# Performance work log

Measured on AMD Instinct MI355X. Metric: run time of the kernel, lower is better.

Reference implementation:

```python
import jax, jax.numpy as jnp
import numpy as np

B, IN, U = 16, 1024, 1024


def _wSw(W, S):
    # W: [i,u], S: [b,i,i] -> W^T S W : [b,u,u]
    return jnp.einsum('iu,bij,jv->buv', W, S, W)


def _xSx(x, Wsig):
    # (sum_i x_i^2) * W_Sigma, broadcast over batch
    return jnp.sum(x * x, axis=1)[:, None, None] * Wsig


def _trS(S, Wsig):
    return jnp.trace(S, axis1=1, axis2=2)[:, None, None] * Wsig


def _hadamard_sigma(s1, s2, m1, m2):
    # s1*s2 + diag(m1) s2 diag(m1) + diag(m2) s1 diag(m2)
    return (s1 * s2
            + m1[:, :, None] * s2 * m1[:, None, :]
            + m2[:, :, None] * s1 * m2[:, None, :])


def _act_sigma(g, S):
    # S * outer(g, g)
    return S * (g[:, :, None] * g[:, None, :])


def setup_inputs() -> dict:
    key = jax.random.key(0)
    ks = jax.random.split(key, 16)
    f32 = jnp.float32
    init_mu, ini_sigma = 0.05, -4.6
    inp = {
        'mu_inputs': jax.random.normal(ks[0], (B, IN), f32),
        'sigma_inputs': 0.01 * jax.random.normal(ks[1], (B, IN, IN), f32),
        'prev_state': 0.1 * jax.random.normal(ks[2], (B, U), f32),
        'Sigma_state': 0.01 * jax.random.normal(ks[3], (B, U, U), f32),
        'U_z': init_mu * jax.random.normal(ks[4], (IN, U), f32),
        'uz_sigma': jnp.full((U,), ini_sigma, f32),
        'W_z': init_mu * jax.random.normal(ks[5], (U, U), f32),
        'wz_sigma': jnp.full((U,), ini_sigma, f32),
        'U_r': init_mu * jax.random.normal(ks[6], (IN, U), f32),
        'ur_sigma': jnp.full((U,), ini_sigma, f32),
        'W_r': init_mu * jax.random.normal(ks[7], (U, U), f32),
        'wr_sigma': jnp.full((U,), ini_sigma, f32),
        'U_h': init_mu * jax.random.normal(ks[8], (IN, U), f32),
        'uh_sigma': jnp.full((U,), ini_sigma, f32),
        'W_h': init_mu * jax.random.normal(ks[9], (U, U), f32),
        'wh_sigma': jnp.full((U,), ini_sigma, f32),
    }
    return inp


def reference(mu_inputs, sigma_inputs, prev_state, Sigma_state,
              U_z, uz_sigma, W_z, wz_sigma,
              U_r, ur_sigma, W_r, wr_sigma,
              U_h, uh_sigma, W_h, wh_sigma):
    sp = jax.nn.softplus
    # ---- z gate ----
    pre_z = mu_inputs @ U_z + prev_state @ W_z
    z = jax.nn.sigmoid(pre_z)
    Uz_S, Wz_S = jnp.diag(sp(uz_sigma)), jnp.diag(sp(wz_sigma))
    Sigma_zz = (_wSw(U_z, sigma_inputs) + _xSx(mu_inputs, Uz_S) + _trS(sigma_inputs, Uz_S)
                + _wSw(W_z, Sigma_state) + _xSx(prev_state, Wz_S) + _trS(Sigma_state, Wz_S))
    Sigma_z = _act_sigma(z * (1.0 - z), Sigma_zz)  # analytic d sigmoid
    # ---- r gate ----
    pre_r = mu_inputs @ U_r + prev_state @ W_r
    r = jax.nn.sigmoid(pre_r)
    Ur_S, Wr_S = jnp.diag(sp(ur_sigma)), jnp.diag(sp(wr_sigma))
    Sigma_rr = (_wSw(U_r, sigma_inputs) + _xSx(mu_inputs, Ur_S) + _trS(sigma_inputs, Ur_S)
                + _wSw(W_r, Sigma_state) + _xSx(prev_state, Wr_S) + _trS(Sigma_state, Wr_S))
    Sigma_r = _act_sigma(r * (1.0 - r), Sigma_rr)
    # ---- h gate ----
    sr = prev_state * r
    pre_h = mu_inputs @ U_h + sr @ W_h
    h = jnp.tanh(pre_h)
    Uh_S, Wh_S = jnp.diag(sp(uh_sigma)), jnp.diag(sp(wh_sigma))
    sigma_g = _hadamard_sigma(Sigma_state, Sigma_r, prev_state, r)
    Sigma_hh = (_wSw(U_h, sigma_inputs) + _xSx(mu_inputs, Uh_S) + _trS(sigma_inputs, Uh_S)
                + _wSw(W_h, sigma_g) + _xSx(sr, Wh_S) + _trS(sigma_g, Wh_S))
    Sigma_h = _act_sigma(1.0 - h * h, Sigma_hh)  # analytic d tanh
    # ---- combine ----
    mu_out = z * prev_state + (1.0 - z) * h
    sigma_a = _hadamard_sigma(Sigma_z, Sigma_state, z, prev_state)
    sigma_b = _hadamard_sigma(Sigma_z, Sigma_h, 1.0 - z, h)
    sigma_ab = Sigma_z * (prev_state[:, :, None] * h[:, None, :])
    sigma_abT = Sigma_z * (h[:, :, None] * prev_state[:, None, :])
    Sigma_out = sigma_a + sigma_b - sigma_ab - sigma_abT
    Sigma_out = jnp.where(jnp.isfinite(Sigma_out), Sigma_out, jnp.zeros_like(Sigma_out))
    eye = jnp.eye(Sigma_out.shape[-1], dtype=bool)
    Sigma_out = jnp.where(eye, jnp.abs(Sigma_out), Sigma_out)
    return mu_out, Sigma_out
```

## Files before the change

kernel.cpp:

```cpp
#include <hip/hip_runtime.h>
#include <math.h>


#define B_  16
#define N_  1024
#define NN_ (1024*1024)

typedef __bf16 bf16x8 __attribute__((ext_vector_type(8)));
typedef float  f32x4  __attribute__((ext_vector_type(4)));
typedef unsigned short ushort8v __attribute__((ext_vector_type(8)));

__device__ __forceinline__ unsigned short f2bf(float f) {
  union { float f; unsigned int u; } v; v.f = f;
  unsigned int r = v.u + 0x7fffu + ((v.u >> 16) & 1u);
  return (unsigned short)(r >> 16);
}
__device__ __forceinline__ float bf2f(unsigned short h) {
  union { unsigned int u; float f; } v; v.u = ((unsigned int)h) << 16;
  return v.f;
}
__device__ __forceinline__ float f4get(const float4& v, int q) {
  return q == 0 ? v.x : (q == 1 ? v.y : (q == 2 ? v.z : v.w));
}
__device__ __forceinline__ unsigned short u4get(const ushort4& v, int q) {
  return q == 0 ? v.x : (q == 1 ? v.y : (q == 2 ? v.z : v.w));
}

__device__ __forceinline__ void gload_lds16(const void* g, void* l) {
  __builtin_amdgcn_global_load_lds((__attribute__((address_space(1))) void*)g,
                                   (__attribute__((address_space(3))) void*)l,
                                   16, 0, 0);
}

template<int OMODE, int PAIR>
__global__ __launch_bounds__(512)
void gemm256(const unsigned short* __restrict__ A, int lda, long aStride, int koffA,
             const unsigned short* __restrict__ Bm, const unsigned short* __restrict__ Bm2,
             int ldb, long bStride, int K,
             void* __restrict__ Out, int ldo, long oStride, int noff,
             const float* __restrict__ act,
             const float* __restrict__ spU, const float* __restrict__ spW,
             const float* __restrict__ dU, const float* __restrict__ dW)
{
  __shared__ unsigned short lds[65536];
  const int b = blockIdx.z;
  const unsigned short* Bsel = Bm;
  int nofx = noff, nbx = blockIdx.x;
  if (PAIR) {
    const int half = gridDim.x >> 1;
    if (nbx >= half) { Bsel = Bm2; nofx = 1024; nbx -= half; }
  }
  const int nbase = nbx * 256;
  const int mbase = blockIdx.y * 256;
  const int t = threadIdx.x, lane = t & 63, w = t >> 6;
  const int wm = w >> 2, wn = w & 3;
  const int NT = K >> 5;

  f32x4 acc[8][4];
  const f32x4 zero4 = {0.f, 0.f, 0.f, 0.f};
#pragma unroll
  for (int i = 0; i < 8; i++)
#pragma unroll
    for (int j = 0; j < 4; j++) acc[i][j] = zero4;

  const int l3 = lane >> 3, l7 = lane & 7;
  const int posg = l7 ^ l3;
  const int gr = ((w * 8 + l3) << 1) + (posg >> 2);
  const int gc = (posg & 3) << 3;
  const unsigned short* Ag = A + (size_t)b * aStride + (size_t)(mbase + gr) * lda + koffA + gc;
  const unsigned short* Bg = Bsel + (size_t)b * bStride + (size_t)(nbase + gr) * ldb + gc;
  const size_t a128 = (size_t)128 * lda, bb128 = (size_t)128 * ldb;
  char* ldsb = (char*)lds;
  const int wdst = w << 10;

  const int lrow = lane & 15, c4 = lane >> 4;
  const int aoff = ((lrow >> 1) << 7) + ((((((lrow & 1) << 2) | c4)) ^ (lrow >> 1)) << 4);
  const int abase0 = (wm << 13);
  const int bbase0 = 16384 + (wn << 12);

  auto STAGE = [&](int kt) {
    const int p = kt & 3;
    const size_t ko = (size_t)kt << 5;
    char* base = ldsb + (p << 15);
    gload_lds16(Ag + ko,          base + wdst);
    gload_lds16(Ag + ko + a128,   base + 8192  + wdst);
    gload_lds16(Bg + ko,          base + 16384 + wdst);
    gload_lds16(Bg + ko + bb128,  base + 24576 + wdst);
  };
  auto LDA8 = [&](const char* pbuf, int mi) -> bf16x8 {
    return *(const bf16x8*)(pbuf + abase0 + (mi << 10) + aoff);
  };
  auto LDB8 = [&](const char* pbuf, int ni) -> bf16x8 {
    return *(const bf16x8*)(pbuf + bbase0 + (ni << 10) + aoff);
  };

  STAGE(0); STAGE(1);
  asm volatile("s_waitcnt vmcnt(4)" ::: "memory");
  __builtin_amdgcn_sched_barrier(0);
  __builtin_amdgcn_s_barrier();
  __builtin_amdgcn_sched_barrier(0);

  bf16x8 a0[4], a1[4], b0[2], b1[2];
#pragma unroll
  for (int i = 0; i < 4; i++) a0[i] = LDA8(ldsb, i);
#pragma unroll
  for (int i = 0; i < 2; i++) b0[i] = LDB8(ldsb, i);

  for (int kt = 0; kt < NT; ++kt) {
    const char* pbuf = ldsb + ((size_t)(kt & 3) << 15);
    const char* pnxt = ldsb + ((size_t)((kt + 1) & 3) << 15);
#pragma unroll
    for (int i = 0; i < 2; i++) b1[i] = LDB8(pbuf, 2 + i);
#pragma unroll
    for (int ni = 0; ni < 2; ni++)
#pragma unroll
      for (int mi = 0; mi < 4; mi++)
        acc[mi][ni] = __builtin_amdgcn_mfma_f32_16x16x32_bf16(a0[mi], b0[ni], acc[mi][ni], 0, 0, 0);
#pragma unroll
    for (int i = 0; i < 4; i++) a1[i] = LDA8(pbuf, 4 + i);
#pragma unroll
    for (int ni = 0; ni < 2; ni++)
#pragma unroll
      for (int mi = 0; mi < 4; mi++)
        acc[mi][2 + ni] = __builtin_amdgcn_mfma_f32_16x16x32_bf16(a0[mi], b1[ni], acc[mi][2 + ni], 0, 0, 0);
    if (kt + 2 < NT) {
      STAGE(kt + 2);
      asm volatile("s_waitcnt vmcnt(4)" ::: "memory");
    } else {
      asm volatile("s_waitcnt vmcnt(0)" ::: "memory");
    }
    __builtin_amdgcn_sched_barrier(0);
    __builtin_amdgcn_s_barrier();
    __builtin_amdgcn_sched_barrier(0);
    if (kt + 1 < NT) {
#pragma unroll
      for (int i = 0; i < 4; i++) a0[i] = LDA8(pnxt, i);
    }
#pragma unroll
    for (int ni = 0; ni < 2; ni++)
#pragma unroll
      for (int mi = 0; mi < 4; mi++)
        acc[4 + mi][ni] = __builtin_amdgcn_mfma_f32_16x16x32_bf16(a1[mi], b0[ni], acc[4 + mi][ni], 0, 0, 0);
    if (kt + 1 < NT) {
#pragma unroll
      for (int i = 0; i < 2; i++) b0[i] = LDB8(pnxt, i);
    }
#pragma unroll
    for (int ni = 0; ni < 2; ni++)
#pragma unroll
      for (int mi = 0; mi < 4; mi++)
        acc[4 + mi][2 + ni] = __builtin_amdgcn_mfma_f32_16x16x32_bf16(a1[mi], b1[ni], acc[4 + mi][2 + ni], 0, 0, 0);
  }

  if (OMODE == 2) {
    const float* actb = act + b * N_;
    const float dUb = dU[b], dWb = dW[b];
#pragma unroll
    for (int mi = 0; mi < 8; mi++) {
      const int u0 = mbase + wm * 128 + mi * 16 + ((lane >> 4) << 2);
#pragma unroll
      for (int ni = 0; ni < 4; ni++) {
        const int v = nbase + wn * 64 + ni * 16 + (lane & 15);
        const float avv = actb[v];
#pragma unroll
        for (int r = 0; r < 4; r++) {
          const int u = u0 + r;
          float val = acc[mi][ni][r];
          if (u == v) val += dUb * spU[u] + dWb * spW[u];
          val *= actb[u] * avv;
          ((float*)Out)[(size_t)b * oStride + (size_t)u * ldo + v] = val;
        }
      }
    }
  } else {
    __syncthreads();
    unsigned short* reg = lds + w * 8192;
    const float* actb = (OMODE == 1) ? (act + b * N_) : nullptr;
    float dUb = 0.f, dWb = 0.f;
    if (OMODE == 1) { dUb = dU[b]; dWb = dW[b]; }
#pragma unroll
    for (int mi = 0; mi < 8; mi++) {
      const int rl0 = mi * 16 + ((lane >> 4) << 2);
#pragma unroll
      for (int ni = 0; ni < 4; ni++) {
        const int cl = ni * 16 + (lane & 15);
#pragma unroll
        for (int r = 0; r < 4; r++) {
          const int rl = rl0 + r;
          float val = acc[mi][ni][r];
          if (OMODE == 1) {
            const int u = mbase + wm * 128 + rl, v = nbase + wn * 64 + cl;
            if (u == v) val += dUb * spU[u] + dWb * spW[u];
            val *= actb[u] * actb[v];
          }
          reg[rl * 64 + cl] = f2bf(val);
        }
      }
    }
    unsigned short* obase = (unsigned short*)Out + (size_t)b * oStride
        + (size_t)(mbase + wm * 128) * ldo + nofx + nbase + wn * 64;
#pragma unroll
    for (int pp = 0; pp < 16; pp++) {
      const int row = pp * 8 + (lane >> 3);
      const int ch = lane & 7;
      ushort8v vv = *(const ushort8v*)&reg[row * 64 + ch * 8];
      *(ushort8v*)(obase + (size_t)row * ldo + ch * 8) = vv;
    }
  }
}


__global__ void conv_bf16(const float* __restrict__ in, unsigned short* __restrict__ out, int n4)
{
  int i = blockIdx.x * 256 + threadIdx.x;
  const int stride = gridDim.x * 256;
  for (; i < n4; i += stride) {
    const float4 v = ((const float4*)in)[i];
    ushort4 o;
    o.x = f2bf(v.x); o.y = f2bf(v.y); o.z = f2bf(v.z); o.w = f2bf(v.w);
    ((ushort4*)out)[i] = o;
  }
}

__global__ void build_AT(const float* __restrict__ Uz, const float* __restrict__ Wz,
                         const float* __restrict__ Ur, const float* __restrict__ Wr,
                         const float* __restrict__ Uh, const float* __restrict__ Wh,
                         unsigned short* __restrict__ AT)
{
  __shared__ float tile[32][33];
  const int g = blockIdx.z;
  const float* U = g == 0 ? Uz : (g == 1 ? Ur : Uh);
  const float* W = g == 0 ? Wz : (g == 1 ? Wr : Wh);
  const int u0  = blockIdx.x * 32;
  const int k0g = blockIdx.y * 32;
  const float* src = (k0g >= 1024) ? W : U;
  const int kloc = k0g & 1023;
  const int tx = threadIdx.x & 31, ty = threadIdx.x >> 5;
  unsigned short* out = AT + (size_t)g * N_ * 2048;
#pragma unroll
  for (int i = 0; i < 32; i += 8) tile[ty + i][tx] = src[(size_t)(kloc + ty + i) * N_ + u0 + tx];
  __syncthreads();
#pragma unroll
  for (int i = 0; i < 32; i += 8)
    out[(size_t)(u0 + ty + i) * 2048 + k0g + tx] = f2bf(tile[tx][ty + i]);
}

__global__ void softplus6(const float* a0, const float* a1, const float* a2,
                          const float* a3, const float* a4, const float* a5,
                          float* __restrict__ sp)
{
  const float* src[6] = {a0, a1, a2, a3, a4, a5};
  const int g = blockIdx.x;
  const float* s = src[g];
  for (int i = threadIdx.x; i < N_; i += 256) {
    float x = s[i];
    sp[g * N_ + i] = (x > 20.f) ? x : log1pf(expf(x));
  }
}

__global__ void scalars1(const float* __restrict__ mu, const float* __restrict__ prev,
                         const float* __restrict__ sin_, const float* __restrict__ Sst,
                         float* __restrict__ dA, float* __restrict__ dBzr)
{
  __shared__ float red[256];
  const int b = blockIdx.x;
  float s1 = 0.f, s2 = 0.f;
  for (int i = threadIdx.x; i < N_; i += 256) {
    const float m = mu[b * N_ + i];
    s1 += m * m + sin_[(size_t)b * NN_ + (size_t)i * (N_ + 1)];
    const float p = prev[b * N_ + i];
    s2 += p * p + Sst[(size_t)b * NN_ + (size_t)i * (N_ + 1)];
  }
  red[threadIdx.x] = s1; __syncthreads();
  for (int s = 128; s > 0; s >>= 1) { if (threadIdx.x < s) red[threadIdx.x] += red[threadIdx.x + s]; __syncthreads(); }
  if (threadIdx.x == 0) dA[b] = red[0];
  __syncthreads();
  red[threadIdx.x] = s2; __syncthreads();
  for (int s = 128; s > 0; s >>= 1) { if (threadIdx.x < s) red[threadIdx.x] += red[threadIdx.x + s]; __syncthreads(); }
  if (threadIdx.x == 0) dBzr[b] = red[0];
}

__global__ __launch_bounds__(256)
void gate_pre2(const float* __restrict__ x1, const float* __restrict__ x2,
               const float* __restrict__ U0, const float* __restrict__ W0,
               const float* __restrict__ U1, const float* __restrict__ W1,
               float* __restrict__ Ppart)
{
  const int g  = blockIdx.z;
  const int ks = blockIdx.y;
  const int out = blockIdx.x * 256 + threadIdx.x;
  const int b = out >> 10, col = out & 1023;
  const float* x = (ks < 4) ? x1 : x2;
  const float* Wm = (g == 0) ? ((ks < 4) ? U0 : W0) : ((ks < 4) ? U1 : W1);
  const int k0 = (ks & 3) * 256;
  const float* xb = x + b * N_ + k0;
  const float* wp = Wm + (size_t)k0 * N_ + col;
  float acc = 0.f;
#pragma unroll 8
  for (int k = 0; k < 256; k++)
    acc += xb[k] * wp[(size_t)k * N_];
  Ppart[(g * 8 + ks) * (B_ * N_) + out] = acc;
}

__global__ void gate_act2(const float* __restrict__ P,
                          float* __restrict__ z, float* __restrict__ gz,
                          float* __restrict__ r, float* __restrict__ gr)
{
  const int out = blockIdx.x * 256 + threadIdx.x;
  float a0 = 0.f, a1 = 0.f;
#pragma unroll
  for (int ks = 0; ks < 8; ks++) {
    a0 += P[ks * (B_ * N_) + out];
    a1 += P[(8 + ks) * (B_ * N_) + out];
  }
  const float s0 = 1.f / (1.f + expf(-a0));
  const float s1 = 1.f / (1.f + expf(-a1));
  z[out] = s0; gz[out] = s0 * (1.f - s0);
  r[out] = s1; gr[out] = s1 * (1.f - s1);
}

__global__ __launch_bounds__(256)
void gate_pre1(const float* __restrict__ x1, const float* __restrict__ x2,
               const float* __restrict__ U0, const float* __restrict__ W0,
               float* __restrict__ Ppart)
{
  const int ks = blockIdx.y;
  const int out = blockIdx.x * 256 + threadIdx.x;
  const int b = out >> 10, col = out & 1023;
  const float* x = (ks < 4) ? x1 : x2;
  const float* Wm = (ks < 4) ? U0 : W0;
  const int k0 = (ks & 3) * 256;
  const float* xb = x + b * N_ + k0;
  const float* wp = Wm + (size_t)k0 * N_ + col;
  float acc = 0.f;
#pragma unroll 8
  for (int k = 0; k < 256; k++)
    acc += xb[k] * wp[(size_t)k * N_];
  Ppart[ks * (B_ * N_) + out] = acc;
}

__global__ void gate_act1(const float* __restrict__ P,
                          float* __restrict__ h, float* __restrict__ gh)
{
  const int out = blockIdx.x * 256 + threadIdx.x;
  float a0 = 0.f;
#pragma unroll
  for (int ks = 0; ks < 8; ks++) a0 += P[ks * (B_ * N_) + out];
  const float s = tanhf(a0);
  h[out] = s; gh[out] = 1.f - s * s;
}

__global__ void sr_csr(const float* __restrict__ prev, const float* __restrict__ r,
                       float* __restrict__ sr, float* __restrict__ csr)
{
  __shared__ float red[256];
  const int b = blockIdx.x;
  float s = 0.f;
  for (int i = threadIdx.x; i < N_; i += 256) {
    const float v = prev[b * N_ + i] * r[b * N_ + i];
    sr[b * N_ + i] = v;
    s += v * v;
  }
  red[threadIdx.x] = s; __syncthreads();
  for (int k = 128; k > 0; k >>= 1) { if (threadIdx.x < k) red[threadIdx.x] += red[threadIdx.x + k]; __syncthreads(); }
  if (threadIdx.x == 0) csr[b] = red[0];
}

__global__ void hadamard_sg(const float* __restrict__ Sst, unsigned short* __restrict__ Sg,
                            const float* __restrict__ prev, const float* __restrict__ r)
{
  const size_t idx = ((size_t)blockIdx.x * 256 + threadIdx.x) * 4;
  const int b = (int)(idx >> 20);
  const int rem = (int)(idx & (NN_ - 1));
  const int i = rem >> 10, j0 = rem & 1023;
  const float pi = prev[b * N_ + i], ri = r[b * N_ + i];
  const float4  ss  = *(const float4*)(Sst + (size_t)b * NN_ + rem);
  const ushort4 sr4 = *(const ushort4*)(Sg + (size_t)b * NN_ + rem);
  ushort4 o;
  unsigned short* op = (unsigned short*)&o;
#pragma unroll
  for (int q = 0; q < 4; q++) {
    const float srv = bf2f(u4get(sr4, q));
    const float stv = f4get(ss, q);
    const float pj = prev[b * N_ + j0 + q];
    const float rj = r[b * N_ + j0 + q];
    op[q] = f2bf(stv * srv + pi * pj * srv + ri * rj * stv);
  }
  *(ushort4*)(Sg + (size_t)b * NN_ + rem) = o;
}

__global__ void scalars2(const unsigned short* __restrict__ Sg,
                         const float* __restrict__ csr, float* __restrict__ dBh)
{
  __shared__ float red[256];
  const int b = blockIdx.x;
  float s = 0.f;
  for (int i = threadIdx.x; i < N_; i += 256)
    s += bf2f(Sg[(size_t)b * NN_ + (size_t)i * (N_ + 1)]);
  red[threadIdx.x] = s; __syncthreads();
  for (int k = 128; k > 0; k >>= 1) { if (threadIdx.x < k) red[threadIdx.x] += red[threadIdx.x + k]; __syncthreads(); }
  if (threadIdx.x == 0) dBh[b] = red[0] + csr[b];
}

__global__ void mu_kernel(const float* __restrict__ z, const float* __restrict__ prev,
                          const float* __restrict__ h, float* __restrict__ mu_out)
{
  const int i = blockIdx.x * 256 + threadIdx.x;
  const float zz = z[i];
  mu_out[i] = zz * prev[i] + (1.f - zz) * h[i];
}

__global__ void combine(const unsigned short* __restrict__ Sz, const float* __restrict__ Sst,
                        const float* __restrict__ z, const float* __restrict__ prev,
                        const float* __restrict__ h, float* __restrict__ SigOut)
{
  const int row = blockIdx.x;
  const int b = row >> 10, u = row & 1023;
  const float zu = z[b * N_ + u], pu = prev[b * N_ + u], hu = h[b * N_ + u];
  const size_t base = (size_t)b * NN_ + (size_t)u * N_;
  const int j0 = threadIdx.x * 4;
  const ushort4 s4 = *(const ushort4*)(Sz + base + j0);
  const float4 sh = *(const float4*)(SigOut + base + j0);
  const float4 st = *(const float4*)(Sst + base + j0);
  const float4 zv = *(const float4*)(z + b * N_ + j0);
  const float4 pv = *(const float4*)(prev + b * N_ + j0);
  const float4 hv = *(const float4*)(h + b * N_ + j0);
  float o[4];
#pragma unroll
  for (int q = 0; q < 4; q++) {
    const int v = j0 + q;
    const float sz  = bf2f(u4get(s4, q));
    const float shh = f4get(sh, q);
    const float stt = f4get(st, q);
    const float zvv = f4get(zv, q);
    const float pvv = f4get(pv, q);
    const float hvv = f4get(hv, q);
    float res = sz * stt + zu * zvv * stt + pu * pvv * sz
              + sz * shh + (1.f - zu) * (1.f - zvv) * shh + hu * hvv * sz
              - sz * (pu * hvv) - sz * (hu * pvv);
    if (!isfinite(res)) res = 0.f;
    if (u == v) res = fabsf(res);
    o[q] = res;
  }
  float4 ov; ov.x = o[0]; ov.y = o[1]; ov.z = o[2]; ov.w = o[3];
  *(float4*)(SigOut + base + j0) = ov;
}


extern "C" void kernel_launch(void* const* d_in, const int* in_sizes, int n_in,
                              void* d_out, int out_size, void* d_ws, size_t ws_size,
                              hipStream_t stream)
{
  const float* mu   = (const float*)d_in[0];
  const float* sin_ = (const float*)d_in[1];
  const float* prev = (const float*)d_in[2];
  const float* Sst  = (const float*)d_in[3];
  const float* Uz = (const float*)d_in[4];  const float* uzs = (const float*)d_in[5];
  const float* Wz = (const float*)d_in[6];  const float* wzs = (const float*)d_in[7];
  const float* Ur = (const float*)d_in[8];  const float* urs = (const float*)d_in[9];
  const float* Wr = (const float*)d_in[10]; const float* wrs = (const float*)d_in[11];
  const float* Uh = (const float*)d_in[12]; const float* uhs = (const float*)d_in[13];
  const float* Wh = (const float*)d_in[14]; const float* whs = (const float*)d_in[15];

  char* ws = (char*)d_ws;
  size_t off = 0;
  auto take = [&](size_t bytes) -> char* {
    char* p = ws + off;
    off = (off + bytes + 255) & ~(size_t)255;
    return p;
  };
  unsigned short* Tcm = (unsigned short*)take((size_t)B_ * 2048 * 1024 * 2);
  unsigned short* Sz  = (unsigned short*)take((size_t)B_ * NN_ * 2);
  unsigned short* Sg  = (unsigned short*)take((size_t)B_ * NN_ * 2);
  unsigned short* AT  = (unsigned short*)take((size_t)3 * N_ * 2048 * 2);
  float* Ppart = (float*)take((size_t)16 * B_ * N_ * 4);
  float* sp   = (float*)take(6 * N_ * 4);
  float* z    = (float*)take(B_ * N_ * 4);
  float* gz   = (float*)take(B_ * N_ * 4);
  float* rr   = (float*)take(B_ * N_ * 4);
  float* gr   = (float*)take(B_ * N_ * 4);
  float* h    = (float*)take(B_ * N_ * 4);
  float* gh   = (float*)take(B_ * N_ * 4);
  float* sr   = (float*)take(B_ * N_ * 4);
  float* dA   = (float*)take(64);
  float* dBzr = (float*)take(64);
  float* dBh  = (float*)take(64);
  float* csr  = (float*)take(64);
  if (off > ws_size) return;

  float* mu_out = (float*)d_out;
  float* SigOut = (float*)d_out + (size_t)B_ * N_;
  unsigned short* SinH = (unsigned short*)SigOut;
  unsigned short* SstH = (unsigned short*)SigOut + (size_t)B_ * NN_;

  const unsigned short* ATz = AT;
  const unsigned short* ATr = AT + (size_t)N_ * 2048;
  const unsigned short* ATh = AT + (size_t)2 * N_ * 2048;

  conv_bf16<<<2048, 256, 0, stream>>>(sin_, SinH, B_ * NN_ / 4);
  conv_bf16<<<2048, 256, 0, stream>>>(Sst,  SstH, B_ * NN_ / 4);
  softplus6<<<6, 256, 0, stream>>>(uzs, wzs, urs, wrs, uhs, whs, sp);
  scalars1<<<16, 256, 0, stream>>>(mu, prev, sin_, Sst, dA, dBzr);
  build_AT<<<dim3(32, 64, 3), 256, 0, stream>>>(Uz, Wz, Ur, Wr, Uh, Wh, AT);
  gate_pre2<<<dim3(64, 8, 2), 256, 0, stream>>>(mu, prev, Uz, Wz, Ur, Wr, Ppart);
  gate_act2<<<64, 256, 0, stream>>>(Ppart, z, gz, rr, gr);
  sr_csr<<<16, 256, 0, stream>>>(prev, rr, sr, csr);
  gate_pre1<<<dim3(64, 8), 256, 0, stream>>>(mu, sr, Uh, Wh, Ppart);
  gate_act1<<<64, 256, 0, stream>>>(Ppart, h, gh);

  const dim3 gg1(8, 4, 16);
  const dim3 gg2(4, 4, 16);
  const long tS = (long)2048 * 1024;

  gemm256<0, 1><<<gg1, 512, 0, stream>>>(ATz, 2048, 0, 0, SinH, SstH, 1024, (long)NN_, 1024,
                                         Tcm, 2048, tS, 0, nullptr, nullptr, nullptr, nullptr, nullptr);
  gemm256<1, 0><<<gg2, 512, 0, stream>>>(ATz, 2048, 0, 0, Tcm, nullptr, 2048, tS, 2048,
                                         Sz, 1024, (long)NN_, 0, gz, sp + 0, sp + 1024, dA, dBzr);
  gemm256<0, 1><<<gg1, 512, 0, stream>>>(ATr, 2048, 0, 0, SinH, SstH, 1024, (long)NN_, 1024,
                                         Tcm, 2048, tS, 0, nullptr, nullptr, nullptr, nullptr, nullptr);
  gemm256<1, 0><<<gg2, 512, 0, stream>>>(ATr, 2048, 0, 0, Tcm, nullptr, 2048, tS, 2048,
                                         Sg, 1024, (long)NN_, 0, gr, sp + 2048, sp + 3072, dA, dBzr);
  hadamard_sg<<<16384, 256, 0, stream>>>(Sst, Sg, prev, rr);
  scalars2<<<16, 256, 0, stream>>>(Sg, csr, dBh);
  gemm256<0, 1><<<gg1, 512, 0, stream>>>(ATh, 2048, 0, 0, SinH, Sg, 1024, (long)NN_, 1024,
                                         Tcm, 2048, tS, 0, nullptr, nullptr, nullptr, nullptr, nullptr);
  gemm256<2, 0><<<gg2, 512, 0, stream>>>(ATh, 2048, 0, 0, Tcm, nullptr, 2048, tS, 2048,
                                         SigOut, 1024, (long)NN_, 0, gh, sp + 4096, sp + 5120, dA, dBh);
  mu_kernel<<<64, 256, 0, stream>>>(z, prev, h, mu_out);
  combine<<<16384, 256, 0, stream>>>(Sz, Sst, z, prev, h, SigOut);
}
```

Before: 584.7 us.

## Rewrite batched GEMM as an 8-phase ping-pong pipeline with XCD-aware block mapping

Replaces the 4-stage, K=32 GEMM with a double-buffered, K=64 tile using 128KB of LDS. Each tile is split into four MFMA phases that interleave LDS reads and half-tile global loads, with barriers and s_setprio around the MFMA bursts. It also switches to a 1D grid that maps panels across XCDs for cache locality, and adds an XOR swizzle to the bf16 epilogue staging to reduce LDS bank conflicts. The paired mode now also offsets the A column by 1024 for the second half, which changes which half of the packed weights multiplies the state covariance. The larger LDS footprint limits occupancy to one block per CU.

```diff
diff --git a/kernel.cpp b/kernel.cpp
--- a/kernel.cpp
+++ b/kernel.cpp
@@ -32,29 +32,33 @@
                                    16, 0, 0);
 }
 
+#define MFMA_ __builtin_amdgcn_mfma_f32_16x16x32_bf16
+
 template<int OMODE, int PAIR>
 __global__ __launch_bounds__(512)
-void gemm256(const unsigned short* __restrict__ A, int lda, long aStride, int koffA,
-             const unsigned short* __restrict__ Bm, const unsigned short* __restrict__ Bm2,
-             int ldb, long bStride, int K,
-             void* __restrict__ Out, int ldo, long oStride, int noff,
-             const float* __restrict__ act,
-             const float* __restrict__ spU, const float* __restrict__ spW,
-             const float* __restrict__ dU, const float* __restrict__ dW)
-{
-  __shared__ unsigned short lds[65536];
-  const int b = blockIdx.z;
-  const unsigned short* Bsel = Bm;
-  int nofx = noff, nbx = blockIdx.x;
-  if (PAIR) {
-    const int half = gridDim.x >> 1;
-    if (nbx >= half) { Bsel = Bm2; nofx = 1024; nbx -= half; }
-  }
-  const int nbase = nbx * 256;
-  const int mbase = blockIdx.y * 256;
-  const int t = threadIdx.x, lane = t & 63, w = t >> 6;
+void gemm8p(const unsigned short* __restrict__ A, int lda, long aStride, int koffA,
+            const unsigned short* __restrict__ Bm, const unsigned short* __restrict__ Bm2,
+            int ldb, long bStride, int K,
+            void* __restrict__ Out, int ldo, long oStride, int noff,
+            const float* __restrict__ act,
+            const float* __restrict__ spU, const float* __restrict__ spW,
+            const float* __restrict__ dU, const float* __restrict__ dW)
+{
+  __shared__ __align__(16) char ldsb[131072];
+  const int id = blockIdx.x;
+  const int xcd = id & 7, rest = id >> 3;
+  const int mt = rest & 3, pp = rest >> 2;
+  const int panel = xcd + (pp << 3);
+  const int nt = panel & 3;
+  const int b  = (panel >> 2) & 15;
+  const int ps = PAIR ? (panel >> 6) : 0;
+  const unsigned short* Bsel = (PAIR && ps) ? Bm2 : Bm;
+  const int kofx = koffA + (ps ? 1024 : 0);
+  const int nofx = noff  + (ps ? 1024 : 0);
+  const int mbase = mt << 8, nbase = nt << 8;
+  const int tid = threadIdx.x, lane = tid & 63, w = tid >> 6;
   const int wm = w >> 2, wn = w & 3;
-  const int NT = K >> 5;
+  const int NT = K >> 6;
 
   f32x4 acc[8][4];
   const f32x4 zero4 = {0.f, 0.f, 0.f, 0.f};
@@ -65,66 +69,113 @@
 
   const int l3 = lane >> 3, l7 = lane & 7;
   const int posg = l7 ^ l3;
-  const int gr = ((w * 8 + l3) << 1) + (posg >> 2);
+  const int gr = (l3 << 1) + (posg >> 2);
   const int gc = (posg & 3) << 3;
-  const unsigned short* Ag = A + (size_t)b * aStride + (size_t)(mbase + gr) * lda + koffA + gc;
-  const unsigned short* Bg = Bsel + (size_t)b * bStride + (size_t)(nbase + gr) * ldb + gc;
-  const size_t a128 = (size_t)128 * lda, bb128 = (size_t)128 * ldb;
-  char* ldsb = (char*)lds;
-  const int wdst = w << 10;
+  const int bi0 = w << 1, bi1 = bi0 + 1;
+  const int rS0 = ((bi0 >> 1) << 4) + gr, cS0 = ((bi0 & 1) << 5) + gc;
+  const int rS1 = ((bi1 >> 1) << 4) + gr, cS1 = ((bi1 & 1) << 5) + gc;
+  const unsigned short* Ab = A + (size_t)b * aStride + (size_t)mbase * lda + kofx;
+  const unsigned short* Bb = Bsel + (size_t)b * bStride + (size_t)nbase * ldb;
+  const int d0 = w << 11, d1 = (w << 11) + 1024;
+
+  auto SA = [&](int tt, int h) {
+    char* dst = ldsb + ((tt & 1) << 16) + (h << 14);
+    const unsigned short* s = Ab + (size_t)(h << 7) * lda + ((size_t)tt << 6);
+    gload_lds16(s + (size_t)rS0 * lda + cS0, dst + d0);
+    gload_lds16(s + (size_t)rS1 * lda + cS1, dst + d1);
+  };
+  auto SB = [&](int tt, int h) {
+    char* dst = ldsb + ((tt & 1) << 16) + 32768 + (h << 14);
+    const unsigned short* s = Bb + (size_t)(h << 7) * ldb + ((size_t)tt << 6);
+    gload_lds16(s + (size_t)rS0 * ldb + cS0, dst + d0);
+    gload_lds16(s + (size_t)rS1 * ldb + cS1, dst + d1);
+  };
 
   const int lrow = lane & 15, c4 = lane >> 4;
-  const int aoff = ((lrow >> 1) << 7) + ((((((lrow & 1) << 2) | c4)) ^ (lrow >> 1)) << 4);
-  const int abase0 = (wm << 13);
-  const int bbase0 = 16384 + (wn << 12);
-
-  auto STAGE = [&](int kt) {
-    const int p = kt & 3;
-    const size_t ko = (size_t)kt << 5;
-    char* base = ldsb + (p << 15);
-    gload_lds16(Ag + ko,          base + wdst);
-    gload_lds16(Ag + ko + a128,   base + 8192  + wdst);
-    gload_lds16(Bg + ko,          base + 16384 + wdst);
-    gload_lds16(Bg + ko + bb128,  base + 24576 + wdst);
+  const int aoff = ((lrow >> 1) << 7) + (((((lrow & 1) << 2) | c4) ^ (lrow >> 1)) << 4);
+  const int abase = wm << 14;
+  const int bbase = 32768 + ((wn >> 1) << 14);
+  const int brg   = (wn & 1) << 2;
+  auto LDA = [&](const char* pb, int mi, int ks) -> bf16x8 {
+    return *(const bf16x8*)(pb + abase + (((mi << 1) + ks) << 10) + aoff);
   };
-  auto LDA8 = [&](const char* pbuf, int mi) -> bf16x8 {
-    return *(const bf16x8*)(pbuf + abase0 + (mi << 10) + aoff);
+  auto LDB = [&](const char* pb, int ni, int ks) -> bf16x8 {
+    return *(const bf16x8*)(pb + bbase + ((((brg + ni) << 1) + ks) << 10) + aoff);
   };
-  auto LDB8 = [&](const char* pbuf, int ni) -> bf16x8 {
-    return *(const bf16x8*)(pbuf + bbase0 + (ni << 10) + aoff);
-  };
-
-  STAGE(0); STAGE(1);
+
+  SA(0, 0); SA(0, 1); SB(0, 0); SB(0, 1);
+  if (NT > 1) { SB(1, 0); SA(1, 0); }
   asm volatile("s_waitcnt vmcnt(4)" ::: "memory");
   __builtin_amdgcn_sched_barrier(0);
   __builtin_amdgcn_s_barrier();
   __builtin_amdgcn_sched_barrier(0);
 
-  bf16x8 a0[4], a1[4], b0[2], b1[2];
-#pragma unroll
-  for (int i = 0; i < 4; i++) a0[i] = LDA8(ldsb, i);
-#pragma unroll
-  for (int i = 0; i < 2; i++) b0[i] = LDB8(ldsb, i);
-
+  bf16x8 av[4][2], bv[4][2];
   for (int kt = 0; kt < NT; ++kt) {
-    const char* pbuf = ldsb + ((size_t)(kt & 3) << 15);
-    const char* pnxt = ldsb + ((size_t)((kt + 1) & 3) << 15);
-#pragma unroll
-    for (int i = 0; i < 2; i++) b1[i] = LDB8(pbuf, 2 + i);
+    const char* pb = ldsb + ((kt & 1) << 16);
+#pragma unroll
+    for (int mi = 0; mi < 4; mi++)
+#pragma unroll
+      for (int ks = 0; ks < 2; ks++) av[mi][ks] = LDA(pb, mi, ks);
 #pragma unroll
     for (int ni = 0; ni < 2; ni++)
 #pragma unroll
-      for (int mi = 0; mi < 4; mi++)
-        acc[mi][ni] = __builtin_amdgcn_mfma_f32_16x16x32_bf16(a0[mi], b0[ni], acc[mi][ni], 0, 0, 0);
-#pragma unroll
-    for (int i = 0; i < 4; i++) a1[i] = LDA8(pbuf, 4 + i);
+      for (int ks = 0; ks < 2; ks++) bv[ni][ks] = LDB(pb, ni, ks);
+    if (kt + 1 < NT) SB(kt + 1, 1);
+    __builtin_amdgcn_s_barrier();
+    asm volatile("s_waitcnt lgkmcnt(0)" ::: "memory");
+    __builtin_amdgcn_sched_barrier(0);
+    __builtin_amdgcn_s_setprio(1);
 #pragma unroll
     for (int ni = 0; ni < 2; ni++)
 #pragma unroll
-      for (int mi = 0; mi < 4; mi++)
-        acc[mi][2 + ni] = __builtin_amdgcn_mfma_f32_16x16x32_bf16(a0[mi], b1[ni], acc[mi][2 + ni], 0, 0, 0);
+      for (int mi = 0; mi < 4; mi++) {
+        acc[mi][ni] = MFMA_(av[mi][0], bv[ni][0], acc[mi][ni], 0, 0, 0);
+        acc[mi][ni] = MFMA_(av[mi][1], bv[ni][1], acc[mi][ni], 0, 0, 0);
+      }
+    __builtin_amdgcn_s_setprio(0);
+    __builtin_amdgcn_sched_barrier(0);
+    __builtin_amdgcn_s_barrier();
+#pragma unroll
+    for (int ni = 2; ni < 4; ni++)
+#pragma unroll
+      for (int ks = 0; ks < 2; ks++) bv[ni][ks] = LDB(pb, ni, ks);
+    if (kt + 1 < NT) SA(kt + 1, 1);
+    __builtin_amdgcn_s_barrier();
+    asm volatile("s_waitcnt lgkmcnt(0)" ::: "memory");
+    __builtin_amdgcn_sched_barrier(0);
+    __builtin_amdgcn_s_setprio(1);
+#pragma unroll
+    for (int ni = 2; ni < 4; ni++)
+#pragma unroll
+      for (int mi = 0; mi < 4; mi++) {
+        acc[mi][ni] = MFMA_(av[mi][0], bv[ni][0], acc[mi][ni], 0, 0, 0);
+        acc[mi][ni] = MFMA_(av[mi][1], bv[ni][1], acc[mi][ni], 0, 0, 0);
+      }
+    __builtin_amdgcn_s_setprio(0);
+    __builtin_amdgcn_sched_barrier(0);
+    __builtin_amdgcn_s_barrier();
+#pragma unroll
+    for (int mi = 0; mi < 4; mi++)
+#pragma unroll
+      for (int ks = 0; ks < 2; ks++) av[mi][ks] = LDA(pb, 4 + mi, ks);
+    if (kt + 2 < NT) SB(kt + 2, 0);
+    __builtin_amdgcn_s_barrier();
+    asm volatile("s_waitcnt lgkmcnt(0)" ::: "memory");
+    __builtin_amdgcn_sched_barrier(0);
+    __builtin_amdgcn_s_setprio(1);
+#pragma unroll
+    for (int ni = 0; ni < 2; ni++)
+#pragma unroll
+      for (int mi = 0; mi < 4; mi++) {
+        acc[4 + mi][ni] = MFMA_(av[mi][0], bv[ni][0], acc[4 + mi][ni], 0, 0, 0);
+        acc[4 + mi][ni] = MFMA_(av[mi][1], bv[ni][1], acc[4 + mi][ni], 0, 0, 0);
+      }
+    __builtin_amdgcn_s_setprio(0);
+    __builtin_amdgcn_sched_barrier(0);
+    __builtin_amdgcn_s_barrier();
     if (kt + 2 < NT) {
-      STAGE(kt + 2);
+      SA(kt + 2, 0);
       asm volatile("s_waitcnt vmcnt(4)" ::: "memory");
     } else {
       asm volatile("s_waitcnt vmcnt(0)" ::: "memory");
@@ -132,24 +183,17 @@
     __builtin_amdgcn_sched_barrier(0);
     __builtin_amdgcn_s_barrier();
     __builtin_amdgcn_sched_barrier(0);
-    if (kt + 1 < NT) {
-#pragma unroll
-      for (int i = 0; i < 4; i++) a0[i] = LDA8(pnxt, i);
-    }
-#pragma unroll
-    for (int ni = 0; ni < 2; ni++)
-#pragma unroll
-      for (int mi = 0; mi < 4; mi++)
-        acc[4 + mi][ni] = __builtin_amdgcn_mfma_f32_16x16x32_bf16(a1[mi], b0[ni], acc[4 + mi][ni], 0, 0, 0);
-    if (kt + 1 < NT) {
-#pragma unroll
-      for (int i = 0; i < 2; i++) b0[i] = LDB8(pnxt, i);
-    }
-#pragma unroll
-    for (int ni = 0; ni < 2; ni++)
-#pragma unroll
-      for (int mi = 0; mi < 4; mi++)
-        acc[4 + mi][2 + ni] = __builtin_amdgcn_mfma_f32_16x16x32_bf16(a1[mi], b1[ni], acc[4 + mi][2 + ni], 0, 0, 0);
+    __builtin_amdgcn_s_setprio(1);
+#pragma unroll
+    for (int ni = 2; ni < 4; ni++)
+#pragma unroll
+      for (int mi = 0; mi < 4; mi++) {
+        acc[4 + mi][ni] = MFMA_(av[mi][0], bv[ni][0], acc[4 + mi][ni], 0, 0, 0);
+        acc[4 + mi][ni] = MFMA_(av[mi][1], bv[ni][1], acc[4 + mi][ni], 0, 0, 0);
+      }
+    __builtin_amdgcn_s_setprio(0);
+    __builtin_amdgcn_sched_barrier(0);
+    __builtin_amdgcn_s_barrier();
   }
 
   if (OMODE == 2) {
@@ -174,7 +218,7 @@
     }
   } else {
     __syncthreads();
-    unsigned short* reg = lds + w * 8192;
+    unsigned short* scr = (unsigned short*)(ldsb + w * 16384);
     const float* actb = (OMODE == 1) ? (act + b * N_) : nullptr;
     float dUb = 0.f, dWb = 0.f;
     if (OMODE == 1) { dUb = dU[b]; dWb = dW[b]; }
@@ -193,18 +237,20 @@
             if (u == v) val += dUb * spU[u] + dWb * spW[u];
             val *= actb[u] * actb[v];
           }
-          reg[rl * 64 + cl] = f2bf(val);
+          scr[rl * 64 + ((((cl >> 3) ^ (rl & 7))) << 3) + (cl & 7)] = f2bf(val);
         }
       }
     }
-    unsigned short* obase = (unsigned short*)Out + (size_t)b * oStride
+    asm volatile("s_waitcnt lgkmcnt(0)" ::: "memory");
+    __builtin_amdgcn_sched_barrier(0);
+    unsigned short* ob = (unsigned short*)Out + (size_t)b * oStride
         + (size_t)(mbase + wm * 128) * ldo + nofx + nbase + wn * 64;
 #pragma unroll
-    for (int pp = 0; pp < 16; pp++) {
-      const int row = pp * 8 + (lane >> 3);
-      const int ch = lane & 7;
-      ushort8v vv = *(const ushort8v*)&reg[row * 64 + ch * 8];
-      *(ushort8v*)(obase + (size_t)row * ldo + ch * 8) = vv;
+    for (int pq = 0; pq < 16; pq++) {
+      const int row = pq * 8 + (lane >> 3);
+      const int ch = (lane & 7) ^ (row & 7);
+      ushort8v vv = *(const ushort8v*)&scr[row * 64 + ((lane & 7) << 3)];
+      *(ushort8v*)(ob + (size_t)row * ldo + ch * 8) = vv;
     }
   }
 }
@@ -508,24 +554,22 @@
   gate_pre1<<<dim3(64, 8), 256, 0, stream>>>(mu, sr, Uh, Wh, Ppart);
   gate_act1<<<64, 256, 0, stream>>>(Ppart, h, gh);
 
-  const dim3 gg1(8, 4, 16);
-  const dim3 gg2(4, 4, 16);
   const long tS = (long)2048 * 1024;
 
-  gemm256<0, 1><<<gg1, 512, 0, stream>>>(ATz, 2048, 0, 0, SinH, SstH, 1024, (long)NN_, 1024,
-                                         Tcm, 2048, tS, 0, nullptr, nullptr, nullptr, nullptr, nullptr);
-  gemm256<1, 0><<<gg2, 512, 0, stream>>>(ATz, 2048, 0, 0, Tcm, nullptr, 2048, tS, 2048,
-                                         Sz, 1024, (long)NN_, 0, gz, sp + 0, sp + 1024, dA, dBzr);
-  gemm256<0, 1><<<gg1, 512, 0, stream>>>(ATr, 2048, 0, 0, SinH, SstH, 1024, (long)NN_, 1024,
-                                         Tcm, 2048, tS, 0, nullptr, nullptr, nullptr, nullptr, nullptr);
-  gemm256<1, 0><<<gg2, 512, 0, stream>>>(ATr, 2048, 0, 0, Tcm, nullptr, 2048, tS, 2048,
-                                         Sg, 1024, (long)NN_, 0, gr, sp + 2048, sp + 3072, dA, dBzr);
+  gemm8p<0, 1><<<512, 512, 0, stream>>>(ATz, 2048, 0, 0, SinH, SstH, 1024, (long)NN_, 1024,
+                                        Tcm, 2048, tS, 0, nullptr, nullptr, nullptr, nullptr, nullptr);
+  gemm8p<1, 0><<<256, 512, 0, stream>>>(ATz, 2048, 0, 0, Tcm, nullptr, 2048, tS, 2048,
+                                        Sz, 1024, (long)NN_, 0, gz, sp + 0, sp + 1024, dA, dBzr);
+  gemm8p<0, 1><<<512, 512, 0, stream>>>(ATr, 2048, 0, 0, SinH, SstH, 1024, (long)NN_, 1024,
+                                        Tcm, 2048, tS, 0, nullptr, nullptr, nullptr, nullptr, nullptr);
+  gemm8p<1, 0><<<256, 512, 0, stream>>>(ATr, 2048, 0, 0, Tcm, nullptr, 2048, tS, 2048,
+                                        Sg, 1024, (long)NN_, 0, gr, sp + 2048, sp + 3072, dA, dBzr);
   hadamard_sg<<<16384, 256, 0, stream>>>(Sst, Sg, prev, rr);
   scalars2<<<16, 256, 0, stream>>>(Sg, csr, dBh);
-  gemm256<0, 1><<<gg1, 512, 0, stream>>>(ATh, 2048, 0, 0, SinH, Sg, 1024, (long)NN_, 1024,
-                                         Tcm, 2048, tS, 0, nullptr, nullptr, nullptr, nullptr, nullptr);
-  gemm256<2, 0><<<gg2, 512, 0, stream>>>(ATh, 2048, 0, 0, Tcm, nullptr, 2048, tS, 2048,
-                                         SigOut, 1024, (long)NN_, 0, gh, sp + 4096, sp + 5120, dA, dBh);
+  gemm8p<0, 1><<<512, 512, 0, stream>>>(ATh, 2048, 0, 0, SinH, Sg, 1024, (long)NN_, 1024,
+                                        Tcm, 2048, tS, 0, nullptr, nullptr, nullptr, nullptr, nullptr);
+  gemm8p<2, 0><<<256, 512, 0, stream>>>(ATh, 2048, 0, 0, Tcm, nullptr, 2048, tS, 2048,
+                                        SigOut, 1024, (long)NN_, 0, gh, sp + 4096, sp + 5120, dA, dBh);
   mu_kernel<<<64, 256, 0, stream>>>(z, prev, h, mu_out);
   combine<<<16384, 256, 0, stream>>>(Sz, Sst, z, prev, h, SigOut);
 }
```

Measured after the change: 568.3 us. -2.8%, faster.
